# Performance work log

Hardware: AMD Instinct MI355X
Metric: run time of the kernel (lower is better)

## Reference

```python
import jax, jax.numpy as jnp
import numpy as np

LN_EPS = 1e-5

def _layernorm(x, gamma, beta):
    mu = jnp.mean(x, axis=-1, keepdims=True)
    var = jnp.mean((x - mu) ** 2, axis=-1, keepdims=True)
    return (x - mu) / jnp.sqrt(var + LN_EPS) * gamma + beta

def setup_inputs() -> dict:
    key = jax.random.key(0)
    ks = jax.random.split(key, 12)
    B, S, D, V, H = 2, 2048, 1024, 32000, 16
    d_ff = 4 * D
    inp = {}
    inp["V"] = jax.random.randint(ks[0], (B, S), 0, V, dtype=jnp.int64)
    inp["num_heads"] = H
    sc = 0.02
    inp["emb"] = jax.random.normal(ks[1], (V, D), dtype=jnp.float32) * sc
    inp["w_o"] = jax.random.normal(ks[2], (D, D), dtype=jnp.float32) * sc
    inp["w1"] = jax.random.normal(ks[3], (D, d_ff), dtype=jnp.float32) * sc
    inp["b1"] = jnp.zeros((d_ff,), dtype=jnp.float32)
    inp["w2"] = jax.random.normal(ks[4], (d_ff, D), dtype=jnp.float32) * sc
    inp["b2"] = jnp.zeros((D,), dtype=jnp.float32)
    inp["gamma1"] = jnp.ones((D,), dtype=jnp.float32)
    inp["beta1"] = jnp.zeros((D,), dtype=jnp.float32)
    inp["gamma2"] = jnp.ones((D,), dtype=jnp.float32)
    inp["beta2"] = jnp.zeros((D,), dtype=jnp.float32)
    return inp

def reference(V, num_heads, emb, w_o, w1, b1, w2, b2, gamma1, beta1, gamma2, beta2):
    # Embedding lookup: [B, S, D]
    x = emb[V]
    B, S, D = x.shape
    hd = D // num_heads
    # NOTE: the original forward never applies w_q/w_k/w_v -- q=k=v=embedding,
    # split per head along the feature dim.
    qh = x.reshape(B, S, num_heads, hd)
    scores = jnp.einsum("bqhd,bkhd->bhqk", qh, qh) / jnp.sqrt(jnp.float32(hd))
    attn = jax.nn.softmax(scores, axis=-1)
    ctx = jnp.einsum("bhqk,bkhd->bqhd", attn, qh).reshape(B, S, D)
    attn_out = ctx @ w_o
    x1 = _layernorm(x + attn_out, gamma1, beta1)
    ff = jax.nn.relu(x1 @ w1 + b1) @ w2 + b2
    return _layernorm(x1 + ff, gamma2, beta2)
```

## Files before the change

### kernel.cpp

```cpp
#include <hip/hip_runtime.h>
#include <hip/hip_bf16.h>

#define B_  2
#define S_  2048
#define D_  1024
#define H_  16
#define HD_ 64
#define DFF 4096
#define NT  (B_ * S_)

typedef __bf16 bf16;
typedef __bf16 bf16x8 __attribute__((ext_vector_type(8)));
typedef __bf16 bf16x4 __attribute__((ext_vector_type(4)));
typedef __bf16 bf16x2 __attribute__((ext_vector_type(2)));
typedef float  f32x4  __attribute__((ext_vector_type(4)));
typedef float  f32x16 __attribute__((ext_vector_type(16)));
typedef int    i32x2  __attribute__((ext_vector_type(2)));

typedef const __attribute__((address_space(1))) unsigned int GLB_U32;
typedef __attribute__((address_space(3))) unsigned int AS3_U32;

__device__ __forceinline__ void gload16(const void* g, void* l) {
    __builtin_amdgcn_global_load_lds((GLB_U32*)g, (AS3_U32*)l, 16, 0, 0);
}

#define MFMA32(A, B, C) __builtin_amdgcn_mfma_f32_32x32x16_bf16(A, B, C, 0, 0, 0)
#define MFMA16(A, B, C) __builtin_amdgcn_mfma_f32_16x16x32_bf16(A, B, C, 0, 0, 0)

__device__ __forceinline__ unsigned pk2(float a, float b) {
    union { bf16x2 v; unsigned u; } t;
    t.v[0] = (bf16)a; t.v[1] = (bf16)b;
    return t.u;
}

#define ATT_SCL 0.18033688011112042f

#define PREP_EMB  (B_ * (S_ / 32) * (D_ / 32))
#define PREP_WO   ((D_ / 32) * (D_ / 32))
#define PREP_W1   ((D_ / 32) * (DFF / 32))
#define PREP_W2   ((DFF / 32) * (D_ / 32))
#define PREP_TOT  (PREP_EMB + PREP_WO + PREP_W1 + PREP_W2)

__device__ __forceinline__ void transcvt_tile(const float* src, bf16* dst,
                                              int R, int C, int tile,
                                              float* tf, int tx, int ty) {
    int tiles_c = C >> 5;
    int r0 = (tile / tiles_c) << 5;
    int c0 = (tile % tiles_c) << 5;
#pragma unroll
    for (int i = 0; i < 4; i++)
        tf[(ty + i * 8) * 33 + tx] = src[(size_t)(r0 + ty + i * 8) * C + c0 + tx];
    __syncthreads();
#pragma unroll
    for (int i = 0; i < 4; i++)
        dst[(size_t)(c0 + ty + i * 8) * R + r0 + tx] = (bf16)tf[tx * 33 + ty + i * 8];
}

__global__ __launch_bounds__(256)
void k_prep(const int* __restrict__ V, const float* __restrict__ emb,
            bf16* __restrict__ xb, bf16* __restrict__ xT,
            const float* __restrict__ w_o, bf16* __restrict__ wobT,
            const float* __restrict__ w1, bf16* __restrict__ w1T,
            const float* __restrict__ w2, bf16* __restrict__ w2T) {
    __shared__ float tf[32 * 33];
    int bidx = blockIdx.x;
    int tx = threadIdx.x & 31, ty = threadIdx.x >> 5;

    if (bidx < PREP_EMB) {
        bf16* tb = (bf16*)tf;
        const int tiles_d = D_ / 32;
        int b   = bidx / ((S_ / 32) * tiles_d);
        int rem = bidx % ((S_ / 32) * tiles_d);
        int ts = rem / tiles_d, td = rem % tiles_d;
        int s0 = ts * 32, d0 = td * 32;
        bf16* xbb = xb + (size_t)b * S_ * D_;
        bf16* dst = xT + (size_t)b * D_ * S_;
#pragma unroll
        for (int i = 0; i < 4; i++) {
            int srow = s0 + ty + i * 8;
            int vid = V[b * S_ + srow];
            bf16 val = (bf16)emb[(size_t)vid * D_ + d0 + tx];
            xbb[(size_t)srow * D_ + d0 + tx] = val;
            tb[(ty + i * 8) * 34 + tx] = val;
        }
        __syncthreads();
#pragma unroll
        for (int i = 0; i < 4; i++)
            dst[(size_t)(d0 + ty + i * 8) * S_ + s0 + tx] = tb[tx * 34 + ty + i * 8];
    } else if (bidx < PREP_EMB + PREP_WO) {
        transcvt_tile(w_o, wobT, D_, D_, bidx - PREP_EMB, tf, tx, ty);
    } else if (bidx < PREP_EMB + PREP_WO + PREP_W1) {
        transcvt_tile(w1, w1T, D_, DFF, bidx - PREP_EMB - PREP_WO, tf, tx, ty);
    } else {
        transcvt_tile(w2, w2T, DFF, D_, bidx - PREP_EMB - PREP_WO - PREP_W1, tf, tx, ty);
    }
}

__global__ __launch_bounds__(256)
void k_attn(const bf16* __restrict__ xb, const bf16* __restrict__ xT,
            bf16* __restrict__ ctxb) {
    __shared__ alignas(16) bf16 Kt[3][64][64];
    __shared__ alignas(16) bf16 Vt[3][64][64];

    int bh = blockIdx.x >> 4;
    int qt = blockIdx.x & 15;
    int b = bh >> 4, h = bh & 15;
    int tid = threadIdx.x;
    int w = tid >> 6, lane = tid & 63;
    int l31 = lane & 31, hi = lane >> 5;

    const bf16* xq = xb + (size_t)b * S_ * D_ + h * HD_;
    const bf16* vT = xT + ((size_t)b * D_ + h * HD_) * S_;

    int q0 = qt * 128 + w * 32;

    bf16x8 qf[4];
#pragma unroll
    for (int c = 0; c < 4; c++) {
        qf[c] = *(const bf16x8*)(xq + (size_t)(q0 + l31) * D_ + c * 16 + hi * 8);
#pragma unroll
        for (int i = 0; i < 8; i++)
            qf[c][i] = (bf16)((float)qf[c][i] * ATT_SCL);
    }

    bf16x8 onesf;
#pragma unroll
    for (int i = 0; i < 8; i++) onesf[i] = (bf16)1.0f;

    int srow = tid >> 3;
    int sbyx = ((tid & 7) << 4) ^ ((srow & 7) << 4);

    const char* kg = (const char*)(xq + (size_t)srow * D_) + sbyx;
    const char* vg = (const char*)(vT + (size_t)srow * S_) + sbyx;

    char* kdA = (char*)&Kt[0][0][0] + tid * 16;
    char* kdB = (char*)&Kt[1][0][0] + tid * 16;
    char* kdC = (char*)&Kt[2][0][0] + tid * 16;
    char* vdA = (char*)&Vt[0][0][0] + tid * 16;
    char* vdB = (char*)&Vt[1][0][0] + tid * 16;
    char* vdC = (char*)&Vt[2][0][0] + tid * 16;

    const int KSTR = 64 * D_ * 2;
    const int VSTR = 64 * 2;
    const int NTILES = S_ / 64;

    auto stage = [&](char* kd, char* vd) {
        gload16(kg, kd); gload16(kg + 32 * D_ * 2, kd + 4096);
        gload16(vg, vd); gload16(vg + 32 * S_ * 2, vd + 4096);
        kg += KSTR; vg += VSTR;
    };

    stage(kdA, vdA);
    stage(kdB, vdB);

    int rsw = (l31 & 7) << 4;
    const char* KrA = (const char*)&Kt[0][0][0] + l31 * 128;
    const char* KrB = (const char*)&Kt[1][0][0] + l31 * 128;
    const char* KrC = (const char*)&Kt[2][0][0] + l31 * 128;
    const char* VrA = (const char*)&Vt[0][0][0] + l31 * 128;
    const char* VrB = (const char*)&Vt[1][0][0] + l31 * 128;
    const char* VrC = (const char*)&Vt[2][0][0] + l31 * 128;

    f32x16 o0 = {}, o1 = {}, ol = {};

    for (int kt = 0; kt < NTILES; kt++) {
        if (kt == NTILES - 1) asm volatile("s_waitcnt vmcnt(0)" ::: "memory");
        else                  asm volatile("s_waitcnt vmcnt(4)" ::: "memory");
        __builtin_amdgcn_s_barrier();
        __builtin_amdgcn_sched_barrier(0);
        if (kt + 2 < NTILES) stage(kdC, vdC);

        const char* Kb = KrA;
        const char* Vb = VrA;

        f32x16 sa0 = {}, sa1 = {};
        {
            bf16x8 kf0[4], kf1[4];
#pragma unroll
            for (int c = 0; c < 4; c++) {
                int by = (c * 32 + hi * 16) ^ rsw;
                kf0[c] = *(const bf16x8*)(Kb + by);
                kf1[c] = *(const bf16x8*)(Kb + 32 * 128 + by);
            }
            __builtin_amdgcn_s_setprio(1);
#pragma unroll
            for (int c = 0; c < 4; c++) sa0 = MFMA32(kf0[c], qf[c], sa0);
#pragma unroll
            for (int c = 0; c < 4; c++) sa1 = MFMA32(kf1[c], qf[c], sa1);
            __builtin_amdgcn_s_setprio(0);
        }

        float p0[16], p1[16];
#pragma unroll
        for (int i = 0; i < 16; i++) p0[i] = exp2f(sa0[i]);
#pragma unroll
        for (int i = 0; i < 16; i++) p1[i] = exp2f(sa1[i]);

        union { unsigned u[4]; bf16x8 v; } pfA0, pfA1, pfB0, pfB1;
        {
            unsigned a0 = pk2(p0[0],  p0[1]),  a1 = pk2(p0[2],  p0[3]);
            unsigned a2 = pk2(p0[4],  p0[5]),  a3 = pk2(p0[6],  p0[7]);
            unsigned a4 = pk2(p0[8],  p0[9]),  a5 = pk2(p0[10], p0[11]);
            unsigned a6 = pk2(p0[12], p0[13]), a7 = pk2(p0[14], p0[15]);
            i32x2 r;
            r = __builtin_amdgcn_permlane32_swap((int)a0, (int)a2, false, false);
            pfA0.u[0] = r[0]; pfA0.u[2] = r[1];
            r = __builtin_amdgcn_permlane32_swap((int)a1, (int)a3, false, false);
            pfA0.u[1] = r[0]; pfA0.u[3] = r[1];
            r = __builtin_amdgcn_permlane32_swap((int)a4, (int)a6, false, false);
            pfA1.u[0] = r[0]; pfA1.u[2] = r[1];
            r = __builtin_amdgcn_permlane32_swap((int)a5, (int)a7, false, false);
            pfA1.u[1] = r[0]; pfA1.u[3] = r[1];
        }
        {
            unsigned a0 = pk2(p1[0],  p1[1]),  a1 = pk2(p1[2],  p1[3]);
            unsigned a2 = pk2(p1[4],  p1[5]),  a3 = pk2(p1[6],  p1[7]);
            unsigned a4 = pk2(p1[8],  p1[9]),  a5 = pk2(p1[10], p1[11]);
            unsigned a6 = pk2(p1[12], p1[13]), a7 = pk2(p1[14], p1[15]);
            i32x2 r;
            r = __builtin_amdgcn_permlane32_swap((int)a0, (int)a2, false, false);
            pfB0.u[0] = r[0]; pfB0.u[2] = r[1];
            r = __builtin_amdgcn_permlane32_swap((int)a1, (int)a3, false, false);
            pfB0.u[1] = r[0]; pfB0.u[3] = r[1];
            r = __builtin_amdgcn_permlane32_swap((int)a4, (int)a6, false, false);
            pfB1.u[0] = r[0]; pfB1.u[2] = r[1];
            r = __builtin_amdgcn_permlane32_swap((int)a5, (int)a7, false, false);
            pfB1.u[1] = r[0]; pfB1.u[3] = r[1];
        }

        {
            bf16x8 v0, v1, v2, v3;
            v0 = *(const bf16x8*)(Vb + ((0  + hi * 16) ^ rsw));
            v1 = *(const bf16x8*)(Vb + ((32 + hi * 16) ^ rsw));
            v2 = *(const bf16x8*)(Vb + ((64 + hi * 16) ^ rsw));
            v3 = *(const bf16x8*)(Vb + ((96 + hi * 16) ^ rsw));
            __builtin_amdgcn_s_setprio(1);
            o0 = MFMA32(v0, pfA0.v, o0);
            o0 = MFMA32(v1, pfA1.v, o0);
            o0 = MFMA32(v2, pfB0.v, o0);
            o0 = MFMA32(v3, pfB1.v, o0);
            ol = MFMA32(onesf, pfA0.v, ol);
            ol = MFMA32(onesf, pfA1.v, ol);
            __builtin_amdgcn_s_setprio(0);
            v0 = *(const bf16x8*)(Vb + 32 * 128 + ((0  + hi * 16) ^ rsw));
            v1 = *(const bf16x8*)(Vb + 32 * 128 + ((32 + hi * 16) ^ rsw));
            v2 = *(const bf16x8*)(Vb + 32 * 128 + ((64 + hi * 16) ^ rsw));
            v3 = *(const bf16x8*)(Vb + 32 * 128 + ((96 + hi * 16) ^ rsw));
            __builtin_amdgcn_s_setprio(1);
            o1 = MFMA32(v0, pfA0.v, o1);
            o1 = MFMA32(v1, pfA1.v, o1);
            o1 = MFMA32(v2, pfB0.v, o1);
            o1 = MFMA32(v3, pfB1.v, o1);
            ol = MFMA32(onesf, pfB0.v, ol);
            ol = MFMA32(onesf, pfB1.v, ol);
            __builtin_amdgcn_s_setprio(0);
        }

        const char* tk = KrA; KrA = KrB; KrB = KrC; KrC = tk;
        const char* tv = VrA; VrA = VrB; VrB = VrC; VrC = tv;
        char* tk2 = kdA; kdA = kdB; kdB = kdC; kdC = tk2;
        char* tv2 = vdA; vdA = vdB; vdB = vdC; vdC = tv2;
    }

    float rinv = 1.0f / ol[0];
    int q = q0 + l31;
    bf16* crow = ctxb + ((size_t)b * S_ + q) * D_ + h * HD_;
#pragma unroll
    for (int g = 0; g < 4; g++) {
        bf16x4 ov;
#pragma unroll
        for (int j = 0; j < 4; j++) ov[j] = (bf16)(o0[4 * g + j] * rinv);
        *(bf16x4*)(crow + 8 * g + 4 * hi) = ov;
    }
#pragma unroll
    for (int g = 0; g < 4; g++) {
        bf16x4 ov;
#pragma unroll
        for (int j = 0; j < 4; j++) ov[j] = (bf16)(o1[4 * g + j] * rinv);
        *(bf16x4*)(crow + 32 + 8 * g + 4 * hi) = ov;
    }
}

template <int BIAS, int RELU, int OUT_MODE, int SPLITK>
__global__ __launch_bounds__(512)
void k_gemm256(const bf16* __restrict__ A, const bf16* __restrict__ Bt,
               const float* __restrict__ bias,
               float* __restrict__ outf, bf16* __restrict__ outb,
               int M, int N, int K) {
    __shared__ alignas(16) bf16 As[2][256][64];
    __shared__ alignas(16) bf16 Bs[2][256][64];

    int ntn = N >> 8;
    int m0 = (int)(blockIdx.x / ntn) << 8;
    int n0 = (int)(blockIdx.x % ntn) << 8;
    int tid = threadIdx.x;
    int lane = tid & 63, w = tid >> 6;
    int wm = w >> 2, wn = w & 3;
    int l15 = lane & 15, lhi = lane >> 4;

    int Ks = K / SPLITK;
    int NK = Ks >> 6;
    size_t kbase = (size_t)blockIdx.y * Ks;
    float* outpf = outf ? outf + (size_t)blockIdx.y * M * N : nullptr;
    bf16*  outpb = outb ? outb + (size_t)blockIdx.y * M * N : nullptr;

    int r0 = tid >> 3;
    int sbyx = ((tid & 7) << 4) ^ ((r0 & 7) << 4);
    const char* ag = (const char*)(A  + (size_t)(m0 + r0) * K + kbase) + sbyx;
    const char* bg = (const char*)(Bt + (size_t)(n0 + r0) * K + kbase) + sbyx;
    const size_t r64 = (size_t)64 * K * 2;

    auto stA = [&](int ob, size_t ko, int half) {
        char* d = (char*)&As[ob][0][0] + half * 16384 + tid * 16;
        gload16(ag + ko + (size_t)(2 * half) * r64, d);
        gload16(ag + ko + (size_t)(2 * half + 1) * r64, d + 8192);
    };
    auto stB = [&](int ob, size_t ko, int half) {
        char* d = (char*)&Bs[ob][0][0] + half * 16384 + tid * 16;
        gload16(bg + ko + (size_t)(2 * half) * r64, d);
        gload16(bg + ko + (size_t)(2 * half + 1) * r64, d + 8192);
    };

    stA(0, 0, 0); stA(0, 0, 1); stB(0, 0, 0); stB(0, 0, 1);

    f32x4 acc[8][4] = {};
    int rsw = (l15 & 7) << 4;
    int aro = (wm * 128 + l15) * 128;
    int bro = (wn * 64 + l15) * 128;

    for (int t = 0; t < NK; t++) {
        int buf = t & 1, ob = buf ^ 1;
        size_t ko = (size_t)(t + 1) * 128;
        const char* aB = (const char*)&As[buf][0][0] + aro;
        const char* bB = (const char*)&Bs[buf][0][0] + bro;
        bf16x8 af[4][2], bfr[4][2];

        if (t + 1 < NK) {
            stA(ob, ko, 0); stA(ob, ko, 1);
            asm volatile("s_waitcnt vmcnt(4)" ::: "memory");
        } else {
            asm volatile("s_waitcnt vmcnt(0)" ::: "memory");
        }
        __builtin_amdgcn_s_barrier();
        __builtin_amdgcn_sched_barrier(0);
#pragma unroll
        for (int mi = 0; mi < 4; mi++) {
            af[mi][0] = *(const bf16x8*)(aB + mi * 2048 + ((lhi * 16) ^ rsw));
            af[mi][1] = *(const bf16x8*)(aB + mi * 2048 + ((64 + lhi * 16) ^ rsw));
        }
#pragma unroll
        for (int ni = 0; ni < 2; ni++) {
            bfr[ni][0] = *(const bf16x8*)(bB + ni * 2048 + ((lhi * 16) ^ rsw));
            bfr[ni][1] = *(const bf16x8*)(bB + ni * 2048 + ((64 + lhi * 16) ^ rsw));
        }
        __builtin_amdgcn_s_setprio(1);
#pragma unroll
        for (int mi = 0; mi < 4; mi++)
#pragma unroll
            for (int ni = 0; ni < 2; ni++) {
                acc[mi][ni] = MFMA16(af[mi][0], bfr[ni][0], acc[mi][ni]);
                acc[mi][ni] = MFMA16(af[mi][1], bfr[ni][1], acc[mi][ni]);
            }
        __builtin_amdgcn_s_setprio(0);
        __builtin_amdgcn_s_barrier();

#pragma unroll
        for (int ni = 2; ni < 4; ni++) {
            bfr[ni][0] = *(const bf16x8*)(bB + ni * 2048 + ((lhi * 16) ^ rsw));
            bfr[ni][1] = *(const bf16x8*)(bB + ni * 2048 + ((64 + lhi * 16) ^ rsw));
        }
        if (t + 1 < NK) { stB(ob, ko, 0); stB(ob, ko, 1); }
        __builtin_amdgcn_s_barrier();
        __builtin_amdgcn_s_setprio(1);
#pragma unroll
        for (int mi = 0; mi < 4; mi++)
#pragma unroll
            for (int ni = 2; ni < 4; ni++) {
                acc[mi][ni] = MFMA16(af[mi][0], bfr[ni][0], acc[mi][ni]);
                acc[mi][ni] = MFMA16(af[mi][1], bfr[ni][1], acc[mi][ni]);
            }
        __builtin_amdgcn_s_setprio(0);
        __builtin_amdgcn_s_barrier();

#pragma unroll
        for (int mi = 0; mi < 4; mi++) {
            af[mi][0] = *(const bf16x8*)(aB + (4 + mi) * 2048 + ((lhi * 16) ^ rsw));
            af[mi][1] = *(const bf16x8*)(aB + (4 + mi) * 2048 + ((64 + lhi * 16) ^ rsw));
        }
        __builtin_amdgcn_s_barrier();
        __builtin_amdgcn_s_setprio(1);
#pragma unroll
        for (int mi = 0; mi < 4; mi++)
#pragma unroll
            for (int ni = 0; ni < 2; ni++) {
                acc[4 + mi][ni] = MFMA16(af[mi][0], bfr[ni][0], acc[4 + mi][ni]);
                acc[4 + mi][ni] = MFMA16(af[mi][1], bfr[ni][1], acc[4 + mi][ni]);
            }
        __builtin_amdgcn_s_setprio(0);
        __builtin_amdgcn_s_barrier();

        __builtin_amdgcn_s_barrier();
        __builtin_amdgcn_s_setprio(1);
#pragma unroll
        for (int mi = 0; mi < 4; mi++)
#pragma unroll
            for (int ni = 2; ni < 4; ni++) {
                acc[4 + mi][ni] = MFMA16(af[mi][0], bfr[ni][0], acc[4 + mi][ni]);
                acc[4 + mi][ni] = MFMA16(af[mi][1], bfr[ni][1], acc[4 + mi][ni]);
            }
        __builtin_amdgcn_s_setprio(0);
        __builtin_amdgcn_s_barrier();
    }

#pragma unroll
    for (int mi = 0; mi < 8; mi++) {
        int grow = m0 + wm * 128 + mi * 16 + lhi * 4;
#pragma unroll
        for (int ni = 0; ni < 4; ni++) {
            int gcol = n0 + wn * 64 + ni * 16 + l15;
            float bv = BIAS ? bias[gcol] : 0.f;
#pragma unroll
            for (int r = 0; r < 4; r++) {
                float v = acc[mi][ni][r] + bv;
                if (RELU) v = fmaxf(v, 0.f);
                size_t idx = (size_t)(grow + r) * N + gcol;
                if (OUT_MODE & 1) outpf[idx] = v;
                if (OUT_MODE & 2) outpb[idx] = (bf16)v;
            }
        }
    }
}

template <int BIAS, int RELU, int OUT_MODE, int SPLITK>
__global__ __launch_bounds__(512)
void k_g2(const bf16* __restrict__ A, const bf16* __restrict__ Bt,
          const float* __restrict__ bias,
          float* __restrict__ outf, bf16* __restrict__ outb,
          int M, int N, int K) {
    __shared__ alignas(16) bf16 As[2][256][64];
    __shared__ alignas(16) bf16 Bs[2][128][64];

    int ntn = N >> 7;
    int m0 = (int)(blockIdx.x / ntn) << 8;
    int n0 = (int)(blockIdx.x % ntn) << 7;
    int tid = threadIdx.x;
    int lane = tid & 63, w = tid >> 6;
    int wm = w >> 1, wn = w & 1;
    int l15 = lane & 15, lhi = lane >> 4;

    int Ks = K / SPLITK;
    int NK = Ks >> 6;
    size_t kbase = (size_t)blockIdx.y * Ks;
    float* outpf = outf ? outf + (size_t)blockIdx.y * M * N : nullptr;
    bf16*  outpb = outb ? outb + (size_t)blockIdx.y * M * N : nullptr;

    int srow = tid >> 3;
    int sbyx = ((tid & 7) << 4) ^ ((srow & 7) << 4);
    const char* ag = (const char*)(A  + (size_t)(m0 + srow) * K + kbase) + sbyx;
    const char* bg = (const char*)(Bt + (size_t)(n0 + srow) * K + kbase) + sbyx;
    const size_t r64 = (size_t)64 * K * 2;

    auto stA = [&](int ob, size_t ko) {
        char* d = (char*)&As[ob][0][0] + tid * 16;
        gload16(ag + ko, d);
        gload16(ag + ko + r64, d + 8192);
        gload16(ag + ko + 2 * r64, d + 16384);
        gload16(ag + ko + 3 * r64, d + 24576);
    };
    auto stB = [&](int ob, size_t ko) {
        char* d = (char*)&Bs[ob][0][0] + tid * 16;
        gload16(bg + ko, d);
        gload16(bg + ko + r64, d + 8192);
    };

    stA(0, 0); stB(0, 0);

    f32x4 acc[4][4] = {};
    int rsw = (l15 & 7) << 4;
    int aro = (wm * 64 + l15) * 128;
    int bro = (wn * 64 + l15) * 128;

    for (int t = 0; t < NK; t++) {
        int buf = t & 1, ob = buf ^ 1;
        size_t ko = (size_t)(t + 1) * 128;
        const char* aB = (const char*)&As[buf][0][0] + aro;
        const char* bB = (const char*)&Bs[buf][0][0] + bro;
        bf16x8 af[4][2], bn[4][2];

        if (t + 1 < NK) {
            stA(ob, ko);
            asm volatile("s_waitcnt vmcnt(2)" ::: "memory");
        } else {
            asm volatile("s_waitcnt vmcnt(0)" ::: "memory");
        }
        __builtin_amdgcn_s_barrier();
        __builtin_amdgcn_sched_barrier(0);
#pragma unroll
        for (int mi = 0; mi < 4; mi++)
            af[mi][0] = *(const bf16x8*)(aB + mi * 2048 + ((lhi * 16) ^ rsw));
#pragma unroll
        for (int ni = 0; ni < 4; ni++)
            bn[ni][0] = *(const bf16x8*)(bB + ni * 2048 + ((lhi * 16) ^ rsw));
        __builtin_amdgcn_s_setprio(1);
#pragma unroll
        for (int mi = 0; mi < 4; mi++)
#pragma unroll
            for (int ni = 0; ni < 4; ni++)
                acc[mi][ni] = MFMA16(af[mi][0], bn[ni][0], acc[mi][ni]);
        __builtin_amdgcn_s_setprio(0);
        __builtin_amdgcn_s_barrier();

#pragma unroll
        for (int mi = 0; mi < 4; mi++)
            af[mi][1] = *(const bf16x8*)(aB + mi * 2048 + ((64 + lhi * 16) ^ rsw));
#pragma unroll
        for (int ni = 0; ni < 4; ni++)
            bn[ni][1] = *(const bf16x8*)(bB + ni * 2048 + ((64 + lhi * 16) ^ rsw));
        if (t + 1 < NK) stB(ob, ko);
        __builtin_amdgcn_s_barrier();
        __builtin_amdgcn_s_setprio(1);
#pragma unroll
        for (int mi = 0; mi < 4; mi++)
#pragma unroll
            for (int ni = 0; ni < 4; ni++)
                acc[mi][ni] = MFMA16(af[mi][1], bn[ni][1], acc[mi][ni]);
        __builtin_amdgcn_s_setprio(0);
        __builtin_amdgcn_s_barrier();
    }

#pragma unroll
    for (int mi = 0; mi < 4; mi++) {
        int grow = m0 + wm * 64 + mi * 16 + lhi * 4;
#pragma unroll
        for (int ni = 0; ni < 4; ni++) {
            int gcol = n0 + wn * 64 + ni * 16 + l15;
            float bv = BIAS ? bias[gcol] : 0.f;
#pragma unroll
            for (int r = 0; r < 4; r++) {
                float v = acc[mi][ni][r] + bv;
                if (RELU) v = fmaxf(v, 0.f);
                size_t idx = (size_t)(grow + r) * N + gcol;
                if (OUT_MODE & 1) outpf[idx] = v;
                if (OUT_MODE & 2) outpb[idx] = (bf16)v;
            }
        }
    }
}

__global__ __launch_bounds__(256)
void k_ln1(const bf16* __restrict__ p, const bf16* __restrict__ resb,
           const float* __restrict__ gamma, const float* __restrict__ beta,
           bf16* __restrict__ x1b) {
    int row = blockIdx.x, tid = threadIdx.x;
    size_t base = (size_t)row * D_ + tid * 4;
    bf16x4 a = *(const bf16x4*)(p + base);
    bf16x4 c = *(const bf16x4*)(p + (size_t)NT * D_ + base);
    bf16x4 rb = *(const bf16x4*)(resb + base);
    float4 v;
    v.x = (float)a[0] + (float)c[0] + (float)rb[0];
    v.y = (float)a[1] + (float)c[1] + (float)rb[1];
    v.z = (float)a[2] + (float)c[2] + (float)rb[2];
    v.w = (float)a[3] + (float)c[3] + (float)rb[3];
    float s  = v.x + v.y + v.z + v.w;
    float sq = v.x * v.x + v.y * v.y + v.z * v.z + v.w * v.w;
#pragma unroll
    for (int m = 1; m < 64; m <<= 1) {
        s  += __shfl_xor(s, m, 64);
        sq += __shfl_xor(sq, m, 64);
    }
    __shared__ float ss[4], ssq[4];
    int w = tid >> 6;
    if ((tid & 63) == 0) { ss[w] = s; ssq[w] = sq; }
    __syncthreads();
    s  = ss[0] + ss[1] + ss[2] + ss[3];
    sq = ssq[0] + ssq[1] + ssq[2] + ssq[3];
    float mu  = s * (1.f / D_);
    float var = sq * (1.f / D_) - mu * mu;
    float rstd = rsqrtf(var + 1e-5f);
    float4 g  = *(const float4*)(gamma + tid * 4);
    float4 bt = *(const float4*)(beta + tid * 4);
    bf16x4 ob;
    ob[0] = (bf16)((v.x - mu) * rstd * g.x + bt.x);
    ob[1] = (bf16)((v.y - mu) * rstd * g.y + bt.y);
    ob[2] = (bf16)((v.z - mu) * rstd * g.z + bt.z);
    ob[3] = (bf16)((v.w - mu) * rstd * g.w + bt.w);
    *(bf16x4*)(x1b + base) = ob;
}

__global__ __launch_bounds__(256)
void k_ln2(const bf16* __restrict__ p, const float* __restrict__ bias,
           const bf16* __restrict__ resb,
           const float* __restrict__ gamma, const float* __restrict__ beta,
           float* __restrict__ out) {
    int row = blockIdx.x, tid = threadIdx.x;
    size_t base = (size_t)row * D_ + tid * 4;
    bf16x4 s0 = *(const bf16x4*)(p + base);
    bf16x4 s1 = *(const bf16x4*)(p + (size_t)NT * D_ + base);
    bf16x4 s2 = *(const bf16x4*)(p + (size_t)2 * NT * D_ + base);
    bf16x4 s3 = *(const bf16x4*)(p + (size_t)3 * NT * D_ + base);
    bf16x4 rb = *(const bf16x4*)(resb + base);
    float4 bb = *(const float4*)(bias + tid * 4);
    float4 v;
    v.x = ((float)s0[0] + (float)s1[0]) + ((float)s2[0] + (float)s3[0]) + (float)rb[0] + bb.x;
    v.y = ((float)s0[1] + (float)s1[1]) + ((float)s2[1] + (float)s3[1]) + (float)rb[1] + bb.y;
    v.z = ((float)s0[2] + (float)s1[2]) + ((float)s2[2] + (float)s3[2]) + (float)rb[2] + bb.z;
    v.w = ((float)s0[3] + (float)s1[3]) + ((float)s2[3] + (float)s3[3]) + (float)rb[3] + bb.w;
    float s  = v.x + v.y + v.z + v.w;
    float sq = v.x * v.x + v.y * v.y + v.z * v.z + v.w * v.w;
#pragma unroll
    for (int m = 1; m < 64; m <<= 1) {
        s  += __shfl_xor(s, m, 64);
        sq += __shfl_xor(sq, m, 64);
    }
    __shared__ float ss[4], ssq[4];
    int w = tid >> 6;
    if ((tid & 63) == 0) { ss[w] = s; ssq[w] = sq; }
    __syncthreads();
    s  = ss[0] + ss[1] + ss[2] + ss[3];
    sq = ssq[0] + ssq[1] + ssq[2] + ssq[3];
    float mu  = s * (1.f / D_);
    float var = sq * (1.f / D_) - mu * mu;
    float rstd = rsqrtf(var + 1e-5f);
    float4 g  = *(const float4*)(gamma + tid * 4);
    float4 bt = *(const float4*)(beta + tid * 4);
    float4 o;
    o.x = (v.x - mu) * rstd * g.x + bt.x;
    o.y = (v.y - mu) * rstd * g.y + bt.y;
    o.z = (v.z - mu) * rstd * g.z + bt.z;
    o.w = (v.w - mu) * rstd * g.w + bt.w;
    *(float4*)(out + base) = o;
}

extern "C" void kernel_launch(void* const* d_in, const int* in_sizes, int n_in,
                              void* d_out, int out_size, void* d_ws, size_t ws_size,
                              hipStream_t stream) {
    const int*   Vi  = (const int*)d_in[0];
    const float* emb = (const float*)d_in[2];
    const float* w_o = (const float*)d_in[3];
    const float* w1  = (const float*)d_in[4];
    const float* b1  = (const float*)d_in[5];
    const float* w2  = (const float*)d_in[6];
    const float* b2  = (const float*)d_in[7];
    const float* g1  = (const float*)d_in[8];
    const float* be1 = (const float*)d_in[9];
    const float* g2  = (const float*)d_in[10];
    const float* be2 = (const float*)d_in[11];
    float* out = (float*)d_out;

    char* ws = (char*)d_ws;
    size_t off = 0;
    auto alloc = [&](size_t bytes) -> void* {
        void* p = ws + off;
        off += (bytes + 255) & ~(size_t)255;
        return p;
    };
    bf16*  xb   = (bf16*)alloc((size_t)NT * D_ * 2);
    bf16*  xT   = (bf16*)alloc((size_t)NT * D_ * 2);
    bf16*  wobT = (bf16*)alloc((size_t)D_ * D_ * 2);
    bf16*  w1T  = (bf16*)alloc((size_t)DFF * D_ * 2);
    bf16*  w2T  = (bf16*)alloc((size_t)D_ * DFF * 2);
    bf16*  ctxb = (bf16*)alloc((size_t)NT * D_ * 2);
    bf16*  x1b  = (bf16*)alloc((size_t)NT * D_ * 2);
    bf16*  h1   = (bf16*)alloc((size_t)NT * DFF * 2);
    bf16*  RB   = (bf16*)alloc((size_t)4 * NT * D_ * 2);
    bf16*  g1pb = RB;
    bf16*  g3pb = RB;

    k_prep<<<PREP_TOT, 256, 0, stream>>>(Vi, emb, xb, xT, w_o, wobT, w1, w1T, w2, w2T);

    k_attn<<<32 * (S_ / 128), 256, 0, stream>>>(xb, xT, ctxb);

    k_g2<0, 0, 2, 2><<<dim3((NT / 256) * (D_ / 128), 2), 512, 0, stream>>>(
        ctxb, wobT, nullptr, nullptr, g1pb, NT, D_, D_);
    k_ln1<<<NT, 256, 0, stream>>>(g1pb, xb, g1, be1, x1b);

    k_gemm256<1, 1, 2, 1><<<(NT / 256) * (DFF / 256), 512, 0, stream>>>(
        x1b, w1T, b1, nullptr, h1, NT, DFF, D_);

    k_gemm256<0, 0, 2, 4><<<dim3((NT / 256) * (D_ / 256), 4), 512, 0, stream>>>(
        h1, w2T, nullptr, nullptr, g3pb, NT, D_, DFF);
    k_ln2<<<NT, 256, 0, stream>>>(g3pb, b2, x1b, g2, be2, out);
}
```

Before: 199.0 us.

## Process 64 queries per wave in attention to double K/V tile reuse

Each attention wave now computes two 32-query sub-tiles (A and B) against every K/V tile staged in shared memory, so a block covers 256 queries and the grid is halved. This reuses each K fragment and V fragment loaded from LDS across twice as many MFMAs, cutting LDS traffic and global staging per unit of work. The cost is roughly double the accumulator and probability registers per thread, which lowers occupancy, and fewer blocks to fill the GPU. The launch bounds now declare one block per CU.

```diff
diff --git a/kernel.cpp b/kernel.cpp
--- a/kernel.cpp
+++ b/kernel.cpp
@@ -96,14 +96,14 @@
     }
 }
 
-__global__ __launch_bounds__(256)
+__global__ __launch_bounds__(256, 1)
 void k_attn(const bf16* __restrict__ xb, const bf16* __restrict__ xT,
             bf16* __restrict__ ctxb) {
     __shared__ alignas(16) bf16 Kt[3][64][64];
     __shared__ alignas(16) bf16 Vt[3][64][64];
 
-    int bh = blockIdx.x >> 4;
-    int qt = blockIdx.x & 15;
+    int bh = blockIdx.x >> 3;
+    int qt = blockIdx.x & 7;
     int b = bh >> 4, h = bh & 15;
     int tid = threadIdx.x;
     int w = tid >> 6, lane = tid & 63;
@@ -112,15 +112,18 @@
     const bf16* xq = xb + (size_t)b * S_ * D_ + h * HD_;
     const bf16* vT = xT + ((size_t)b * D_ + h * HD_) * S_;
 
-    int q0 = qt * 128 + w * 32;
-
-    bf16x8 qf[4];
+    int q0 = qt * 256 + w * 64;
+
+    bf16x8 qfA[4], qfB[4];
 #pragma unroll
     for (int c = 0; c < 4; c++) {
-        qf[c] = *(const bf16x8*)(xq + (size_t)(q0 + l31) * D_ + c * 16 + hi * 8);
-#pragma unroll
-        for (int i = 0; i < 8; i++)
-            qf[c][i] = (bf16)((float)qf[c][i] * ATT_SCL);
+        qfA[c] = *(const bf16x8*)(xq + (size_t)(q0 + l31) * D_ + c * 16 + hi * 8);
+        qfB[c] = *(const bf16x8*)(xq + (size_t)(q0 + 32 + l31) * D_ + c * 16 + hi * 8);
+#pragma unroll
+        for (int i = 0; i < 8; i++) {
+            qfA[c][i] = (bf16)((float)qfA[c][i] * ATT_SCL);
+            qfB[c][i] = (bf16)((float)qfB[c][i] * ATT_SCL);
+        }
     }
 
     bf16x8 onesf;
@@ -161,7 +164,8 @@
     const char* VrB = (const char*)&Vt[1][0][0] + l31 * 128;
     const char* VrC = (const char*)&Vt[2][0][0] + l31 * 128;
 
-    f32x16 o0 = {}, o1 = {}, ol = {};
+    f32x16 oA0 = {}, oA1 = {}, olA = {};
+    f32x16 oB0 = {}, oB1 = {}, olB = {};
 
     for (int kt = 0; kt < NTILES; kt++) {
         if (kt == NTILES - 1) asm volatile("s_waitcnt vmcnt(0)" ::: "memory");
@@ -173,59 +177,93 @@
         const char* Kb = KrA;
         const char* Vb = VrA;
 
-        f32x16 sa0 = {}, sa1 = {};
+        f32x16 sA0 = {}, sA1 = {}, sB0 = {}, sB1 = {};
         {
-            bf16x8 kf0[4], kf1[4];
+            __builtin_amdgcn_s_setprio(1);
 #pragma unroll
             for (int c = 0; c < 4; c++) {
                 int by = (c * 32 + hi * 16) ^ rsw;
-                kf0[c] = *(const bf16x8*)(Kb + by);
-                kf1[c] = *(const bf16x8*)(Kb + 32 * 128 + by);
+                bf16x8 k0 = *(const bf16x8*)(Kb + by);
+                bf16x8 k1 = *(const bf16x8*)(Kb + 32 * 128 + by);
+                sA0 = MFMA32(k0, qfA[c], sA0);
+                sA1 = MFMA32(k1, qfA[c], sA1);
+                sB0 = MFMA32(k0, qfB[c], sB0);
+                sB1 = MFMA32(k1, qfB[c], sB1);
             }
-            __builtin_amdgcn_s_setprio(1);
-#pragma unroll
-            for (int c = 0; c < 4; c++) sa0 = MFMA32(kf0[c], qf[c], sa0);
-#pragma unroll
-            for (int c = 0; c < 4; c++) sa1 = MFMA32(kf1[c], qf[c], sa1);
             __builtin_amdgcn_s_setprio(0);
         }
 
-        float p0[16], p1[16];
-#pragma unroll
-        for (int i = 0; i < 16; i++) p0[i] = exp2f(sa0[i]);
-#pragma unroll
-        for (int i = 0; i < 16; i++) p1[i] = exp2f(sa1[i]);
-
-        union { unsigned u[4]; bf16x8 v; } pfA0, pfA1, pfB0, pfB1;
+        float pA0[16], pA1[16], pB0[16], pB1[16];
+#pragma unroll
+        for (int i = 0; i < 16; i++) pA0[i] = exp2f(sA0[i]);
+#pragma unroll
+        for (int i = 0; i < 16; i++) pA1[i] = exp2f(sA1[i]);
+#pragma unroll
+        for (int i = 0; i < 16; i++) pB0[i] = exp2f(sB0[i]);
+#pragma unroll
+        for (int i = 0; i < 16; i++) pB1[i] = exp2f(sB1[i]);
+
+        union u4v { unsigned u[4]; bf16x8 v; };
+        u4v pfA[4], pfB[4];
         {
-            unsigned a0 = pk2(p0[0],  p0[1]),  a1 = pk2(p0[2],  p0[3]);
-            unsigned a2 = pk2(p0[4],  p0[5]),  a3 = pk2(p0[6],  p0[7]);
-            unsigned a4 = pk2(p0[8],  p0[9]),  a5 = pk2(p0[10], p0[11]);
-            unsigned a6 = pk2(p0[12], p0[13]), a7 = pk2(p0[14], p0[15]);
+            unsigned a0 = pk2(pA0[0],  pA0[1]),  a1 = pk2(pA0[2],  pA0[3]);
+            unsigned a2 = pk2(pA0[4],  pA0[5]),  a3 = pk2(pA0[6],  pA0[7]);
+            unsigned a4 = pk2(pA0[8],  pA0[9]),  a5 = pk2(pA0[10], pA0[11]);
+            unsigned a6 = pk2(pA0[12], pA0[13]), a7 = pk2(pA0[14], pA0[15]);
             i32x2 r;
             r = __builtin_amdgcn_permlane32_swap((int)a0, (int)a2, false, false);
-            pfA0.u[0] = r[0]; pfA0.u[2] = r[1];
+            pfA[0].u[0] = r[0]; pfA[0].u[2] = r[1];
             r = __builtin_amdgcn_permlane32_swap((int)a1, (int)a3, false, false);
-            pfA0.u[1] = r[0]; pfA0.u[3] = r[1];
+            pfA[0].u[1] = r[0]; pfA[0].u[3] = r[1];
             r = __builtin_amdgcn_permlane32_swap((int)a4, (int)a6, false, false);
-            pfA1.u[0] = r[0]; pfA1.u[2] = r[1];
+            pfA[1].u[0] = r[0]; pfA[1].u[2] = r[1];
             r = __builtin_amdgcn_permlane32_swap((int)a5, (int)a7, false, false);
-            pfA1.u[1] = r[0]; pfA1.u[3] = r[1];
+            pfA[1].u[1] = r[0]; pfA[1].u[3] = r[1];
         }
         {
-            unsigned a0 = pk2(p1[0],  p1[1]),  a1 = pk2(p1[2],  p1[3]);
-            unsigned a2 = pk2(p1[4],  p1[5]),  a3 = pk2(p1[6],  p1[7]);
-            unsigned a4 = pk2(p1[8],  p1[9]),  a5 = pk2(p1[10], p1[11]);
-            unsigned a6 = pk2(p1[12], p1[13]), a7 = pk2(p1[14], p1[15]);
+            unsigned a0 = pk2(pA1[0],  pA1[1]),  a1 = pk2(pA1[2],  pA1[3]);
+            unsigned a2 = pk2(pA1[4],  pA1[5]),  a3 = pk2(pA1[6],  pA1[7]);
+            unsigned a4 = pk2(pA1[8],  pA1[9]),  a5 = pk2(pA1[10], pA1[11]);
+            unsigned a6 = pk2(pA1[12], pA1[13]), a7 = pk2(pA1[14], pA1[15]);
             i32x2 r;
             r = __builtin_amdgcn_permlane32_swap((int)a0, (int)a2, false, false);
-            pfB0.u[0] = r[0]; pfB0.u[2] = r[1];
+            pfA[2].u[0] = r[0]; pfA[2].u[2] = r[1];
             r = __builtin_amdgcn_permlane32_swap((int)a1, (int)a3, false, false);
-            pfB0.u[1] = r[0]; pfB0.u[3] = r[1];
+            pfA[2].u[1] = r[0]; pfA[2].u[3] = r[1];
             r = __builtin_amdgcn_permlane32_swap((int)a4, (int)a6, false, false);
-            pfB1.u[0] = r[0]; pfB1.u[2] = r[1];
+            pfA[3].u[0] = r[0]; pfA[3].u[2] = r[1];
             r = __builtin_amdgcn_permlane32_swap((int)a5, (int)a7, false, false);
-            pfB1.u[1] = r[0]; pfB1.u[3] = r[1];
+            pfA[3].u[1] = r[0]; pfA[3].u[3] = r[1];
+        }
+        {
+            unsigned a0 = pk2(pB0[0],  pB0[1]),  a1 = pk2(pB0[2],  pB0[3]);
+            unsigned a2 = pk2(pB0[4],  pB0[5]),  a3 = pk2(pB0[6],  pB0[7]);
+            unsigned a4 = pk2(pB0[8],  pB0[9]),  a5 = pk2(pB0[10], pB0[11]);
+            unsigned a6 = pk2(pB0[12], pB0[13]), a7 = pk2(pB0[14], pB0[15]);
+            i32x2 r;
+            r = __builtin_amdgcn_permlane32_swap((int)a0, (int)a2, false, false);
+            pfB[0].u[0] = r[0]; pfB[0].u[2] = r[1];
+            r = __builtin_amdgcn_permlane32_swap((int)a1, (int)a3, false, false);
+            pfB[0].u[1] = r[0]; pfB[0].u[3] = r[1];
+            r = __builtin_amdgcn_permlane32_swap((int)a4, (int)a6, false, false);
+            pfB[1].u[0] = r[0]; pfB[1].u[2] = r[1];
+            r = __builtin_amdgcn_permlane32_swap((int)a5, (int)a7, false, false);
+            pfB[1].u[1] = r[0]; pfB[1].u[3] = r[1];
+        }
+        {
+            unsigned a0 = pk2(pB1[0],  pB1[1]),  a1 = pk2(pB1[2],  pB1[3]);
+            unsigned a2 = pk2(pB1[4],  pB1[5]),  a3 = pk2(pB1[6],  pB1[7]);
+            unsigned a4 = pk2(pB1[8],  pB1[9]),  a5 = pk2(pB1[10], pB1[11]);
+            unsigned a6 = pk2(pB1[12], pB1[13]), a7 = pk2(pB1[14], pB1[15]);
+            i32x2 r;
+            r = __builtin_amdgcn_permlane32_swap((int)a0, (int)a2, false, false);
+            pfB[2].u[0] = r[0]; pfB[2].u[2] = r[1];
+            r = __builtin_amdgcn_permlane32_swap((int)a1, (int)a3, false, false);
+            pfB[2].u[1] = r[0]; pfB[2].u[3] = r[1];
+            r = __builtin_amdgcn_permlane32_swap((int)a4, (int)a6, false, false);
+            pfB[3].u[0] = r[0]; pfB[3].u[2] = r[1];
+            r = __builtin_amdgcn_permlane32_swap((int)a5, (int)a7, false, false);
+            pfB[3].u[1] = r[0]; pfB[3].u[3] = r[1];
         }
 
         {
@@ -235,24 +273,36 @@
             v2 = *(const bf16x8*)(Vb + ((64 + hi * 16) ^ rsw));
             v3 = *(const bf16x8*)(Vb + ((96 + hi * 16) ^ rsw));
             __builtin_amdgcn_s_setprio(1);
-            o0 = MFMA32(v0, pfA0.v, o0);
-            o0 = MFMA32(v1, pfA1.v, o0);
-            o0 = MFMA32(v2, pfB0.v, o0);
-            o0 = MFMA32(v3, pfB1.v, o0);
-            ol = MFMA32(onesf, pfA0.v, ol);
-            ol = MFMA32(onesf, pfA1.v, ol);
+            oA0 = MFMA32(v0, pfA[0].v, oA0);
+            oA0 = MFMA32(v1, pfA[1].v, oA0);
+            oA0 = MFMA32(v2, pfA[2].v, oA0);
+            oA0 = MFMA32(v3, pfA[3].v, oA0);
+            oB0 = MFMA32(v0, pfB[0].v, oB0);
+            oB0 = MFMA32(v1, pfB[1].v, oB0);
+            oB0 = MFMA32(v2, pfB[2].v, oB0);
+            oB0 = MFMA32(v3, pfB[3].v, oB0);
+            olA = MFMA32(onesf, pfA[0].v, olA);
+            olA = MFMA32(onesf, pfA[1].v, olA);
+            olA = MFMA32(onesf, pfA[2].v, olA);
+            olA = MFMA32(onesf, pfA[3].v, olA);
             __builtin_amdgcn_s_setprio(0);
             v0 = *(const bf16x8*)(Vb + 32 * 128 + ((0  + hi * 16) ^ rsw));
             v1 = *(const bf16x8*)(Vb + 32 * 128 + ((32 + hi * 16) ^ rsw));
             v2 = *(const bf16x8*)(Vb + 32 * 128 + ((64 + hi * 16) ^ rsw));
             v3 = *(const bf16x8*)(Vb + 32 * 128 + ((96 + hi * 16) ^ rsw));
             __builtin_amdgcn_s_setprio(1);
-            o1 = MFMA32(v0, pfA0.v, o1);
-            o1 = MFMA32(v1, pfA1.v, o1);
-            o1 = MFMA32(v2, pfB0.v, o1);
-            o1 = MFMA32(v3, pfB1.v, o1);
-            ol = MFMA32(onesf, pfB0.v, ol);
-            ol = MFMA32(onesf, pfB1.v, ol);
+            oA1 = MFMA32(v0, pfA[0].v, oA1);
+            oA1 = MFMA32(v1, pfA[1].v, oA1);
+            oA1 = MFMA32(v2, pfA[2].v, oA1);
+            oA1 = MFMA32(v3, pfA[3].v, oA1);
+            oB1 = MFMA32(v0, pfB[0].v, oB1);
+            oB1 = MFMA32(v1, pfB[1].v, oB1);
+            oB1 = MFMA32(v2, pfB[2].v, oB1);
+            oB1 = MFMA32(v3, pfB[3].v, oB1);
+            olB = MFMA32(onesf, pfB[0].v, olB);
+            olB = MFMA32(onesf, pfB[1].v, olB);
+            olB = MFMA32(onesf, pfB[2].v, olB);
+            olB = MFMA32(onesf, pfB[3].v, olB);
             __builtin_amdgcn_s_setprio(0);
         }
 
@@ -262,22 +312,43 @@
         char* tv2 = vdA; vdA = vdB; vdB = vdC; vdC = tv2;
     }
 
-    float rinv = 1.0f / ol[0];
-    int q = q0 + l31;
-    bf16* crow = ctxb + ((size_t)b * S_ + q) * D_ + h * HD_;
-#pragma unroll
-    for (int g = 0; g < 4; g++) {
-        bf16x4 ov;
-#pragma unroll
-        for (int j = 0; j < 4; j++) ov[j] = (bf16)(o0[4 * g + j] * rinv);
-        *(bf16x4*)(crow + 8 * g + 4 * hi) = ov;
-    }
-#pragma unroll
-    for (int g = 0; g < 4; g++) {
-        bf16x4 ov;
-#pragma unroll
-        for (int j = 0; j < 4; j++) ov[j] = (bf16)(o1[4 * g + j] * rinv);
-        *(bf16x4*)(crow + 32 + 8 * g + 4 * hi) = ov;
+    {
+        float rinv = 1.0f / olA[0];
+        int q = q0 + l31;
+        bf16* crow = ctxb + ((size_t)b * S_ + q) * D_ + h * HD_;
+#pragma unroll
+        for (int g = 0; g < 4; g++) {
+            bf16x4 ov;
+#pragma unroll
+            for (int j = 0; j < 4; j++) ov[j] = (bf16)(oA0[4 * g + j] * rinv);
+            *(bf16x4*)(crow + 8 * g + 4 * hi) = ov;
+        }
+#pragma unroll
+        for (int g = 0; g < 4; g++) {
+            bf16x4 ov;
+#pragma unroll
+            for (int j = 0; j < 4; j++) ov[j] = (bf16)(oA1[4 * g + j] * rinv);
+            *(bf16x4*)(crow + 32 + 8 * g + 4 * hi) = ov;
+        }
+    }
+    {
+        float rinv = 1.0f / olB[0];
+        int q = q0 + 32 + l31;
+        bf16* crow = ctxb + ((size_t)b * S_ + q) * D_ + h * HD_;
+#pragma unroll
+        for (int g = 0; g < 4; g++) {
+            bf16x4 ov;
+#pragma unroll
+            for (int j = 0; j < 4; j++) ov[j] = (bf16)(oB0[4 * g + j] * rinv);
+            *(bf16x4*)(crow + 8 * g + 4 * hi) = ov;
+        }
+#pragma unroll
+        for (int g = 0; g < 4; g++) {
+            bf16x4 ov;
+#pragma unroll
+            for (int j = 0; j < 4; j++) ov[j] = (bf16)(oB1[4 * g + j] * rinv);
+            *(bf16x4*)(crow + 32 + 8 * g + 4 * hi) = ov;
+        }
     }
 }
 
@@ -668,7 +739,7 @@
 
     k_prep<<<PREP_TOT, 256, 0, stream>>>(Vi, emb, xb, xT, w_o, wobT, w1, w1T, w2, w2T);
 
-    k_attn<<<32 * (S_ / 128), 256, 0, stream>>>(xb, xT, ctxb);
+    k_attn<<<32 * (S_ / 256), 256, 0, stream>>>(xb, xT, ctxb);
 
     k_g2<0, 0, 2, 2><<<dim3((NT / 256) * (D_ / 128), 2), 512, 0, stream>>>(
         ctxb, wobT, nullptr, nullptr, g1pb, NT, D_, D_);
```

Measured after the change: 211.6 us. 1.06x slower.

## Software-pipeline attention loop to overlap next-tile QK with current softmax-PV

Applied to the files above, without the earlier changes.

Restructures the attention key loop into prologue, steady state and epilogue. Each iteration computes QK scores for the next tile while doing exp, repacking and the PV MFMAs for the previous tile, with V fragments preloaded from LDS. This aims to hide the exp/permlane latency and LDS read latency behind MFMA work. In exchange it raises register pressure from the extra live score and V fragments, and adds an lgkmcnt wait at each barrier.

```diff
diff --git a/kernel.cpp b/kernel.cpp
--- a/kernel.cpp
+++ b/kernel.cpp
@@ -31,6 +31,24 @@
     union { bf16x2 v; unsigned u; } t;
     t.v[0] = (bf16)a; t.v[1] = (bf16)b;
     return t.u;
+}
+
+__device__ __forceinline__ void repack16(const float* p, bf16x8& lo, bf16x8& hiv) {
+    unsigned a0 = pk2(p[0],  p[1]),  a1 = pk2(p[2],  p[3]);
+    unsigned a2 = pk2(p[4],  p[5]),  a3 = pk2(p[6],  p[7]);
+    unsigned a4 = pk2(p[8],  p[9]),  a5 = pk2(p[10], p[11]);
+    unsigned a6 = pk2(p[12], p[13]), a7 = pk2(p[14], p[15]);
+    union { unsigned u[4]; bf16x8 v; } f0, f1;
+    i32x2 r;
+    r = __builtin_amdgcn_permlane32_swap((int)a0, (int)a2, false, false);
+    f0.u[0] = r[0]; f0.u[2] = r[1];
+    r = __builtin_amdgcn_permlane32_swap((int)a1, (int)a3, false, false);
+    f0.u[1] = r[0]; f0.u[3] = r[1];
+    r = __builtin_amdgcn_permlane32_swap((int)a4, (int)a6, false, false);
+    f1.u[0] = r[0]; f1.u[2] = r[1];
+    r = __builtin_amdgcn_permlane32_swap((int)a5, (int)a7, false, false);
+    f1.u[1] = r[0]; f1.u[3] = r[1];
+    lo = f0.v; hiv = f1.v;
 }
 
 #define ATT_SCL 0.18033688011112042f
@@ -162,10 +180,52 @@
     const char* VrC = (const char*)&Vt[2][0][0] + l31 * 128;
 
     f32x16 o0 = {}, o1 = {}, ol = {};
-
-    for (int kt = 0; kt < NTILES; kt++) {
-        if (kt == NTILES - 1) asm volatile("s_waitcnt vmcnt(0)" ::: "memory");
-        else                  asm volatile("s_waitcnt vmcnt(4)" ::: "memory");
+    f32x16 saC0, saC1;
+    bf16x8 vf0, vf1, vf2, vf3, vf4, vf5, vf6, vf7;
+
+    asm volatile("s_waitcnt vmcnt(4)" ::: "memory");
+    __builtin_amdgcn_s_barrier();
+    __builtin_amdgcn_sched_barrier(0);
+    stage(kdC, vdC);
+    {
+        const char* Kb = KrA;
+        const char* Vb = VrA;
+        bf16x8 kf0[4], kf1[4];
+#pragma unroll
+        for (int c = 0; c < 4; c++) {
+            int by = (c * 32 + hi * 16) ^ rsw;
+            kf0[c] = *(const bf16x8*)(Kb + by);
+            kf1[c] = *(const bf16x8*)(Kb + 32 * 128 + by);
+        }
+        f32x16 s0 = {}, s1 = {};
+        __builtin_amdgcn_s_setprio(1);
+#pragma unroll
+        for (int c = 0; c < 4; c++) s0 = MFMA32(kf0[c], qf[c], s0);
+#pragma unroll
+        for (int c = 0; c < 4; c++) s1 = MFMA32(kf1[c], qf[c], s1);
+        __builtin_amdgcn_s_setprio(0);
+        saC0 = s0; saC1 = s1;
+        vf0 = *(const bf16x8*)(Vb + ((0  + hi * 16) ^ rsw));
+        vf1 = *(const bf16x8*)(Vb + ((32 + hi * 16) ^ rsw));
+        vf2 = *(const bf16x8*)(Vb + ((64 + hi * 16) ^ rsw));
+        vf3 = *(const bf16x8*)(Vb + ((96 + hi * 16) ^ rsw));
+        vf4 = *(const bf16x8*)(Vb + 32 * 128 + ((0  + hi * 16) ^ rsw));
+        vf5 = *(const bf16x8*)(Vb + 32 * 128 + ((32 + hi * 16) ^ rsw));
+        vf6 = *(const bf16x8*)(Vb + 32 * 128 + ((64 + hi * 16) ^ rsw));
+        vf7 = *(const bf16x8*)(Vb + 32 * 128 + ((96 + hi * 16) ^ rsw));
+    }
+    {
+        const char* tk = KrA; KrA = KrB; KrB = KrC; KrC = tk;
+        const char* tv = VrA; VrA = VrB; VrB = VrC; VrC = tv;
+        char* tk2 = kdA; kdA = kdB; kdB = kdC; kdC = tk2;
+        char* tv2 = vdA; vdA = vdB; vdB = vdC; vdC = tv2;
+    }
+
+    for (int kt = 1; kt < NTILES; kt++) {
+        if (kt == NTILES - 1)
+            asm volatile("s_waitcnt vmcnt(0) lgkmcnt(0)" ::: "memory");
+        else
+            asm volatile("s_waitcnt vmcnt(4) lgkmcnt(0)" ::: "memory");
         __builtin_amdgcn_s_barrier();
         __builtin_amdgcn_sched_barrier(0);
         if (kt + 2 < NTILES) stage(kdC, vdC);
@@ -173,7 +233,7 @@
         const char* Kb = KrA;
         const char* Vb = VrA;
 
-        f32x16 sa0 = {}, sa1 = {};
+        f32x16 sN0 = {}, sN1 = {};
         {
             bf16x8 kf0[4], kf1[4];
 #pragma unroll
@@ -184,82 +244,76 @@
             }
             __builtin_amdgcn_s_setprio(1);
 #pragma unroll
-            for (int c = 0; c < 4; c++) sa0 = MFMA32(kf0[c], qf[c], sa0);
-#pragma unroll
-            for (int c = 0; c < 4; c++) sa1 = MFMA32(kf1[c], qf[c], sa1);
+            for (int c = 0; c < 4; c++) sN0 = MFMA32(kf0[c], qf[c], sN0);
+#pragma unroll
+            for (int c = 0; c < 4; c++) sN1 = MFMA32(kf1[c], qf[c], sN1);
             __builtin_amdgcn_s_setprio(0);
         }
 
         float p0[16], p1[16];
 #pragma unroll
-        for (int i = 0; i < 16; i++) p0[i] = exp2f(sa0[i]);
-#pragma unroll
-        for (int i = 0; i < 16; i++) p1[i] = exp2f(sa1[i]);
-
-        union { unsigned u[4]; bf16x8 v; } pfA0, pfA1, pfB0, pfB1;
-        {
-            unsigned a0 = pk2(p0[0],  p0[1]),  a1 = pk2(p0[2],  p0[3]);
-            unsigned a2 = pk2(p0[4],  p0[5]),  a3 = pk2(p0[6],  p0[7]);
-            unsigned a4 = pk2(p0[8],  p0[9]),  a5 = pk2(p0[10], p0[11]);
-            unsigned a6 = pk2(p0[12], p0[13]), a7 = pk2(p0[14], p0[15]);
-            i32x2 r;
-            r = __builtin_amdgcn_permlane32_swap((int)a0, (int)a2, false, false);
-            pfA0.u[0] = r[0]; pfA0.u[2] = r[1];
-            r = __builtin_amdgcn_permlane32_swap((int)a1, (int)a3, false, false);
-            pfA0.u[1] = r[0]; pfA0.u[3] = r[1];
-            r = __builtin_amdgcn_permlane32_swap((int)a4, (int)a6, false, false);
-            pfA1.u[0] = r[0]; pfA1.u[2] = r[1];
-            r = __builtin_amdgcn_permlane32_swap((int)a5, (int)a7, false, false);
-            pfA1.u[1] = r[0]; pfA1.u[3] = r[1];
-        }
-        {
-            unsigned a0 = pk2(p1[0],  p1[1]),  a1 = pk2(p1[2],  p1[3]);
-            unsigned a2 = pk2(p1[4],  p1[5]),  a3 = pk2(p1[6],  p1[7]);
-            unsigned a4 = pk2(p1[8],  p1[9]),  a5 = pk2(p1[10], p1[11]);
-            unsigned a6 = pk2(p1[12], p1[13]), a7 = pk2(p1[14], p1[15]);
-            i32x2 r;
-            r = __builtin_amdgcn_permlane32_swap((int)a0, (int)a2, false, false);
-            pfB0.u[0] = r[0]; pfB0.u[2] = r[1];
-            r = __builtin_amdgcn_permlane32_swap((int)a1, (int)a3, false, false);
-            pfB0.u[1] = r[0]; pfB0.u[3] = r[1];
-            r = __builtin_amdgcn_permlane32_swap((int)a4, (int)a6, false, false);
-            pfB1.u[0] = r[0]; pfB1.u[2] = r[1];
-            r = __builtin_amdgcn_permlane32_swap((int)a5, (int)a7, false, false);
-            pfB1.u[1] = r[0]; pfB1.u[3] = r[1];
-        }
-
-        {
-            bf16x8 v0, v1, v2, v3;
-            v0 = *(const bf16x8*)(Vb + ((0  + hi * 16) ^ rsw));
-            v1 = *(const bf16x8*)(Vb + ((32 + hi * 16) ^ rsw));
-            v2 = *(const bf16x8*)(Vb + ((64 + hi * 16) ^ rsw));
-            v3 = *(const bf16x8*)(Vb + ((96 + hi * 16) ^ rsw));
-            __builtin_amdgcn_s_setprio(1);
-            o0 = MFMA32(v0, pfA0.v, o0);
-            o0 = MFMA32(v1, pfA1.v, o0);
-            o0 = MFMA32(v2, pfB0.v, o0);
-            o0 = MFMA32(v3, pfB1.v, o0);
-            ol = MFMA32(onesf, pfA0.v, ol);
-            ol = MFMA32(onesf, pfA1.v, ol);
-            __builtin_amdgcn_s_setprio(0);
-            v0 = *(const bf16x8*)(Vb + 32 * 128 + ((0  + hi * 16) ^ rsw));
-            v1 = *(const bf16x8*)(Vb + 32 * 128 + ((32 + hi * 16) ^ rsw));
-            v2 = *(const bf16x8*)(Vb + 32 * 128 + ((64 + hi * 16) ^ rsw));
-            v3 = *(const bf16x8*)(Vb + 32 * 128 + ((96 + hi * 16) ^ rsw));
-            __builtin_amdgcn_s_setprio(1);
-            o1 = MFMA32(v0, pfA0.v, o1);
-            o1 = MFMA32(v1, pfA1.v, o1);
-            o1 = MFMA32(v2, pfB0.v, o1);
-            o1 = MFMA32(v3, pfB1.v, o1);
-            ol = MFMA32(onesf, pfB0.v, ol);
-            ol = MFMA32(onesf, pfB1.v, ol);
-            __builtin_amdgcn_s_setprio(0);
-        }
+        for (int i = 0; i < 16; i++) p0[i] = exp2f(saC0[i]);
+#pragma unroll
+        for (int i = 0; i < 16; i++) p1[i] = exp2f(saC1[i]);
+        bf16x8 pfA0, pfA1, pfB0, pfB1;
+        repack16(p0, pfA0, pfA1);
+        repack16(p1, pfB0, pfB1);
+
+        __builtin_amdgcn_s_setprio(1);
+        o0 = MFMA32(vf0, pfA0, o0);
+        o0 = MFMA32(vf1, pfA1, o0);
+        o0 = MFMA32(vf2, pfB0, o0);
+        o0 = MFMA32(vf3, pfB1, o0);
+        ol = MFMA32(onesf, pfA0, ol);
+        ol = MFMA32(onesf, pfA1, ol);
+        o1 = MFMA32(vf4, pfA0, o1);
+        o1 = MFMA32(vf5, pfA1, o1);
+        o1 = MFMA32(vf6, pfB0, o1);
+        o1 = MFMA32(vf7, pfB1, o1);
+        ol = MFMA32(onesf, pfB0, ol);
+        ol = MFMA32(onesf, pfB1, ol);
+        __builtin_amdgcn_s_setprio(0);
+
+        vf0 = *(const bf16x8*)(Vb + ((0  + hi * 16) ^ rsw));
+        vf1 = *(const bf16x8*)(Vb + ((32 + hi * 16) ^ rsw));
+        vf2 = *(const bf16x8*)(Vb + ((64 + hi * 16) ^ rsw));
+        vf3 = *(const bf16x8*)(Vb + ((96 + hi * 16) ^ rsw));
+        vf4 = *(const bf16x8*)(Vb + 32 * 128 + ((0  + hi * 16) ^ rsw));
+        vf5 = *(const bf16x8*)(Vb + 32 * 128 + ((32 + hi * 16) ^ rsw));
+        vf6 = *(const bf16x8*)(Vb + 32 * 128 + ((64 + hi * 16) ^ rsw));
+        vf7 = *(const bf16x8*)(Vb + 32 * 128 + ((96 + hi * 16) ^ rsw));
+
+        saC0 = sN0; saC1 = sN1;
 
         const char* tk = KrA; KrA = KrB; KrB = KrC; KrC = tk;
         const char* tv = VrA; VrA = VrB; VrB = VrC; VrC = tv;
         char* tk2 = kdA; kdA = kdB; kdB = kdC; kdC = tk2;
         char* tv2 = vdA; vdA = vdB; vdB = vdC; vdC = tv2;
+    }
+
+    {
+        float p0[16], p1[16];
+#pragma unroll
+        for (int i = 0; i < 16; i++) p0[i] = exp2f(saC0[i]);
+#pragma unroll
+        for (int i = 0; i < 16; i++) p1[i] = exp2f(saC1[i]);
+        bf16x8 pfA0, pfA1, pfB0, pfB1;
+        repack16(p0, pfA0, pfA1);
+        repack16(p1, pfB0, pfB1);
+        __builtin_amdgcn_s_setprio(1);
+        o0 = MFMA32(vf0, pfA0, o0);
+        o0 = MFMA32(vf1, pfA1, o0);
+        o0 = MFMA32(vf2, pfB0, o0);
+        o0 = MFMA32(vf3, pfB1, o0);
+        ol = MFMA32(onesf, pfA0, ol);
+        ol = MFMA32(onesf, pfA1, ol);
+        o1 = MFMA32(vf4, pfA0, o1);
+        o1 = MFMA32(vf5, pfA1, o1);
+        o1 = MFMA32(vf6, pfB0, o1);
+        o1 = MFMA32(vf7, pfB1, o1);
+        ol = MFMA32(onesf, pfB0, ol);
+        ol = MFMA32(onesf, pfB1, ol);
+        __builtin_amdgcn_s_setprio(0);
     }
 
     float rinv = 1.0f / ol[0];
```

Result: no change. 197.2 us (-0.9%).
